# Optimization experiments

Hardware: AMD Instinct MI355X
Metric: run time of the kernel (lower is better)

Reference implementation:

```python
import jax, jax.numpy as jnp
import numpy as np

D_HID = 512
N_HEADS = 16
D_HEAD = D_HID // N_HEADS  # 32
D_FFN = 2048
B, N = 4, 1024
FACTOR = 0.5 / np.sqrt(D_HEAD)
EPS = 1e-5


def layer_norm(x, g, b):
    m = x.mean(-1, keepdims=True)
    v = ((x - m) ** 2).mean(-1, keepdims=True)
    return (x - m) / jnp.sqrt(v + EPS) * g + b


def setup_inputs() -> dict:
    key = jax.random.key(0)
    ks = jax.random.split(key, 24)
    s = 0.02
    p = lambda k, shape: jax.random.normal(k, shape, jnp.float32) * s
    inp = {
        'H': jax.random.normal(ks[0], (B, N, D_HID), jnp.float32),
        'V': jax.random.normal(ks[1], (B, N, 3, D_HID), jnp.float32),
        'D_batch': jax.random.normal(ks[2], (B, N, N), jnp.float32),
        'rbf_bias': jax.random.normal(ks[3], (B, 1, N, N), jnp.float32),
        'H_mask': jax.random.randint(ks[4], (B, N), 0, 2, jnp.int32),
        # attention sublayer params
        'g1': jnp.ones((D_HID,), jnp.float32), 'beta1': jnp.zeros((D_HID,), jnp.float32),
        'Wq': p(ks[5], (D_HID, 4 * D_HID)), 'bq': p(ks[6], (4 * D_HID,)),
        'Wk': p(ks[7], (D_HID, 4 * D_HID)), 'bk': p(ks[8], (4 * D_HID,)),
        'Wv': p(ks[9], (D_HID, D_HID)), 'bv': p(ks[10], (D_HID,)),
        'Wvv': p(ks[11], (D_HID, D_HID)),
        'Wo': p(ks[12], (D_HID, D_HID)), 'bo': p(ks[13], (D_HID,)),
        'Wvo': p(ks[14], (D_HID, D_HID)),
        # GVP FFN sublayer params
        'g2': jnp.ones((D_HID,), jnp.float32), 'beta2': jnp.zeros((D_HID,), jnp.float32),
        'Wlv': p(ks[15], (D_HID, 2 * D_HID)),
        'W1': p(ks[16], (2 * D_HID, D_FFN)), 'b1f': p(ks[17], (D_FFN,)),
        'W2': p(ks[18], (D_FFN, 2 * D_HID)), 'b2f': p(ks[19], (2 * D_HID,)),
    }
    return inp


def ept_forward(H, V, D_batch, rbf_bias, H_mask, g1, beta1, Wq, bq, Wk, bk, Wv, bv,
                Wvv, Wo, bo, Wvo, g2, beta2, Wlv, W1, b1f, W2, b2f):
    b, n, d = H.shape
    # ---- attention sublayer (pre-LN on H only, residual on H and V) ----
    Hn = layer_norm(H, g1, beta1)
    Hq = (Hn @ Wq + bq).reshape(b, n, N_HEADS, 4 * D_HEAD)
    Hk = (Hn @ Wk + bk).reshape(b, n, N_HEADS, 4 * D_HEAD)
    Hv = (Hn @ Wv + bv).reshape(b, n, N_HEADS, D_HEAD)
    # vector values: [b,n,3,d] -> [b,n,heads,3*dh]
    Vv = (V @ Wvv).reshape(b, n, 3, N_HEADS, D_HEAD).transpose(0, 1, 3, 2, 4)
    Vv = Vv.reshape(b, n, N_HEADS, 3 * D_HEAD)
    V_attn = jnp.concatenate([Hv, Vv], axis=-1)  # [b,n,h,4*dh]
    bias = rbf_bias + D_batch[:, None]  # [b,1,n,n]
    keep = (H_mask != 0)[:, None, None, :]  # mask keys
    bias = jnp.where(keep, bias, -jnp.inf)
    logits = jnp.einsum('bnhd,bmhd->bhnm', Hq, Hk) * FACTOR + bias
    attn = jax.nn.softmax(logits, axis=-1)
    res = jnp.einsum('bhnm,bmhd->bnhd', attn, V_attn)  # [b,n,h,4*dh]
    H_res = res[..., :D_HEAD].reshape(b, n, d)
    V_res = res[..., D_HEAD:].reshape(b, n, N_HEADS, 3, D_HEAD)
    V_res = V_res.transpose(0, 1, 3, 2, 4).reshape(b, n, 3, d)
    H = H + H_res @ Wo + bo
    V = V + V_res @ Wvo
    # ---- GVP FFN sublayer (pre-LN on H only, residual) ----
    Hn2 = layer_norm(H, g2, beta2)
    Vp = V @ Wlv  # [b,n,3,2d]
    V1, V2 = Vp[..., :d], Vp[..., d:]
    scaler = jnp.concatenate([Hn2, jnp.sqrt((V1 ** 2).sum(axis=-2))], axis=-1)
    h = jax.nn.silu(scaler @ W1 + b1f) @ W2 + b2f  # [b,n,2d]
    H = H + h[..., :d]
    V = V + h[..., None, d:] * V2
    return H, V


def reference(H, V, D_batch, rbf_bias, H_mask, g1, beta1, Wq, bq, Wk, bk, Wv, bv,
              Wvv, Wo, bo, Wvo, g2, beta2, Wlv, W1, b1f, W2, b2f):
    return ept_forward(H, V, D_batch, rbf_bias, H_mask, g1, beta1, Wq, bq, Wk, bk,
                       Wv, bv, Wvv, Wo, bo, Wvo, g2, beta2, Wlv, W1, b1f, W2, b2f)
```

## Files before the change

kernel.cpp:

```cpp
#include <hip/hip_runtime.h>
#include <math.h>

#define NBATCH 4
#define NSEQ   1024
#define DHID   512
#define NHEADS 16
#define ROWS   (NBATCH*NSEQ)
#define VROWS  (ROWS*3)
#define ATT_FACTOR 0.08838834764831845f
#define LOG2E 1.4426950408889634f
#define F2 (ATT_FACTOR*LOG2E)
#define SM_SHIFT (16.0f*LOG2E)

typedef __attribute__((ext_vector_type(8))) short short8;
typedef __attribute__((ext_vector_type(4))) float floatx4;

#define AS1 __attribute__((address_space(1)))
#define AS3 __attribute__((address_space(3)))
#define GLOAD_LDS16(g, l) \
  __builtin_amdgcn_global_load_lds((const AS1 void*)(g), (AS3 void*)(l), 16, 0, 0)

__device__ __forceinline__ ushort f2bf(float x) {
  union { float f; unsigned u; } v; v.f = x;
  unsigned r = v.u + 0x7fff + ((v.u >> 16) & 1);
  return (ushort)(r >> 16);
}
__device__ __forceinline__ float bf2f(ushort u) {
  union { unsigned u; float f; } v; v.u = ((unsigned)u) << 16; return v.f;
}

template<int OBF>
__global__ __launch_bounds__(256) void ln_kernel(
    const float* __restrict__ x, void* __restrict__ y, int ystride,
    const float* __restrict__ g, const float* __restrict__ beta)
{
  int row = blockIdx.x;
  int t = threadIdx.x;
  const float* xr = x + (size_t)row * DHID;
  float2 v = ((const float2*)xr)[t];
  float s  = v.x + v.y;
  float ss = v.x*v.x + v.y*v.y;
  #pragma unroll
  for (int off = 32; off > 0; off >>= 1) {
    s  += __shfl_down(s, off);
    ss += __shfl_down(ss, off);
  }
  __shared__ float red[8];
  int w = t >> 6;
  if ((t & 63) == 0) { red[w*2] = s; red[w*2+1] = ss; }
  __syncthreads();
  s  = red[0] + red[2] + red[4] + red[6];
  ss = red[1] + red[3] + red[5] + red[7];
  float mean = s * (1.0f/DHID);
  float var  = ss * (1.0f/DHID) - mean*mean;
  float rstd = rsqrtf(var + 1e-5f);
  float2 gg = ((const float2*)g)[t];
  float2 bb = ((const float2*)beta)[t];
  float2 o;
  o.x = (v.x - mean) * rstd * gg.x + bb.x;
  o.y = (v.y - mean) * rstd * gg.y + bb.y;
  if constexpr (OBF) {
    ushort2 u = { f2bf(o.x), f2bf(o.y) };
    *(ushort2*)&((ushort*)y)[(size_t)row * ystride + 2*t] = u;
  } else {
    *(float2*)&((float*)y)[(size_t)row * ystride + 2*t] = o;
  }
}

struct WJobs {
  const float* src[9];
  ushort*      dst[9];
  int K[9];
  int N[9];
  int blk0[10];
};

__global__ __launch_bounds__(256) void wtrans_all_kernel(WJobs J)
{
  __shared__ float Ts[64][65];
  int bid = blockIdx.x;
  int j = 0;
  #pragma unroll
  for (int i = 1; i < 9; i++) if (bid >= J.blk0[i]) j = i;
  const float* W = J.src[j];
  ushort* Wt = J.dst[j];
  int K = J.K[j], N = J.N[j];
  int local = bid - J.blk0[j];
  int nx = N >> 6;
  int bx = local - (local / nx) * nx;
  int by = local / nx;
  int k0 = by*64, n0 = bx*64;
  int t = threadIdx.x;
  #pragma unroll
  for (int p = 0; p < 4; p++) {
    int f = p*256 + t;
    int r = f >> 4, c = (f & 15)*4;
    float4 v = *(const float4*)&W[(size_t)(k0+r)*N + n0 + c];
    Ts[r][c] = v.x; Ts[r][c+1] = v.y; Ts[r][c+2] = v.z; Ts[r][c+3] = v.w;
  }
  __syncthreads();
  #pragma unroll
  for (int p = 0; p < 2; p++) {
    int gidx = p*256 + t;
    int nr = gidx >> 3, kc = (gidx & 7)*8;
    ushort u[8];
    #pragma unroll
    for (int x = 0; x < 8; x++) u[x] = f2bf(Ts[kc+x][nr]);
    ushort4 a = {u[0],u[1],u[2],u[3]}, b4 = {u[4],u[5],u[6],u[7]};
    *(ushort4*)&Wt[(size_t)(n0+nr)*K + k0 + kc]     = a;
    *(ushort4*)&Wt[(size_t)(n0+nr)*K + k0 + kc + 4] = b4;
  }
}

__global__ __launch_bounds__(256) void conv_bf16_kernel(
    const float* __restrict__ x, ushort* __restrict__ y)
{
  int i = blockIdx.x*256 + threadIdx.x;
  float4 v = ((const float4*)x)[i];
  ushort4 u = { f2bf(v.x), f2bf(v.y), f2bf(v.z), f2bf(v.w) };
  ((ushort4*)y)[i] = u;
}

__global__ __launch_bounds__(256) void biascat_kernel(
    const float* __restrict__ bq, const float* __restrict__ bk,
    const float* __restrict__ bv, float* __restrict__ o)
{
  int i = blockIdx.x*256 + threadIdx.x;
  float v = (i < 2048) ? bq[i] : (i < 4096 ? bk[i-2048] : bv[i-4096]);
  o[i] = v;
}

template<int ACT, int HAS_BIAS, int HAS_RES, int OUT_BF16, int DUAL>
__global__ __launch_bounds__(256) void gemm_mfma_kernel(
    const ushort* __restrict__ A, const ushort* __restrict__ Bt,
    const float* __restrict__ bias, const float* __restrict__ resid,
    void* __restrict__ Cv, ushort* __restrict__ C2,
    int M, int N, int K)
{
  __shared__ ushort As[2][128*32];
  __shared__ ushort Bs[2][128*32];
  int t = threadIdx.x;
  int w = t >> 6, lane = t & 63;
  int q16 = lane & 15, quad = lane >> 4;
  int m0 = blockIdx.y * 128, n0 = blockIdx.x * 128;
  int wm = (w & 1) * 64, wn = (w >> 1) * 64;

  int r0 = t >> 2;
  int c0 = (t & 3) * 8;
  const ushort* Ag = A  + (size_t)(m0 + r0) * K + c0;
  const ushort* Bg = Bt + (size_t)(n0 + r0) * K + c0;
  int wb = w * 512;

  floatx4 acc[4][4];
  #pragma unroll
  for (int i = 0; i < 4; i++)
    #pragma unroll
    for (int j = 0; j < 4; j++) acc[i][j] = (floatx4){0.f,0.f,0.f,0.f};

  #define STAGE(buf, kk) do { \
    GLOAD_LDS16(Ag + (kk),                 &As[buf][wb]); \
    GLOAD_LDS16(Ag + (size_t)64*K + (kk),  &As[buf][2048 + wb]); \
    GLOAD_LDS16(Bg + (kk),                 &Bs[buf][wb]); \
    GLOAD_LDS16(Bg + (size_t)64*K + (kk),  &Bs[buf][2048 + wb]); \
  } while (0)

  STAGE(0, 0);
  __syncthreads();

  int nt = K >> 5;
  int cur = 0;
  for (int kt = 0; kt < nt; kt++) {
    if (kt + 1 < nt) STAGE(cur ^ 1, (kt + 1) * 32);
    short8 af[4], bf4[4];
    #pragma unroll
    for (int i = 0; i < 4; i++) {
      af[i]  = *(const short8*)&As[cur][(wm + i*16 + q16)*32 + quad*8];
      bf4[i] = *(const short8*)&Bs[cur][(wn + i*16 + q16)*32 + quad*8];
    }
    #pragma unroll
    for (int i = 0; i < 4; i++)
      #pragma unroll
      for (int j = 0; j < 4; j++)
        acc[i][j] = __builtin_amdgcn_mfma_f32_16x16x32_bf16(af[i], bf4[j], acc[i][j], 0, 0, 0);
    __syncthreads();
    cur ^= 1;
  }
  #undef STAGE

  float* Cf = (float*)Cv;
  ushort* Cu = (ushort*)Cv;
  float bj[4];
  #pragma unroll
  for (int j = 0; j < 4; j++)
    bj[j] = HAS_BIAS ? bias[n0 + wn + j*16 + q16] : 0.f;
  #pragma unroll
  for (int i = 0; i < 4; i++) {
    #pragma unroll
    for (int r = 0; r < 4; r++) {
      int row = m0 + wm + i*16 + quad*4 + r;
      size_t base = (size_t)row * N;
      #pragma unroll
      for (int j = 0; j < 4; j++) {
        int col = n0 + wn + j*16 + q16;
        float v = acc[i][j][r] + bj[j];
        if constexpr (ACT == 1) v = v / (1.f + __expf(-v));
        if constexpr (HAS_RES) v += resid[base + col];
        if constexpr (OUT_BF16) Cu[base + col] = f2bf(v);
        else                    Cf[base + col] = v;
        if constexpr (DUAL) C2[base + col] = f2bf(v);
      }
    }
  }
}

__global__ __launch_bounds__(256) void gemm_wovo_kernel(
    const ushort* __restrict__ A,
    const ushort* __restrict__ WoTp, const ushort* __restrict__ WvoTp,
    const float* __restrict__ bo,
    const float* __restrict__ Hres, const float* __restrict__ Vres,
    float* __restrict__ Hout, float* __restrict__ Vout,
    ushort* __restrict__ Voutbf)
{
  const int K = 512;
  __shared__ ushort As[2][128*32];
  __shared__ ushort Bs[2][128*32];
  int t = threadIdx.x;
  int w = t >> 6, lane = t & 63;
  int q16 = lane & 15, quad = lane >> 4;
  int m0 = blockIdx.y * 128, n0 = blockIdx.x * 128;
  int wm = (w & 1) * 64, wn = (w >> 1) * 64;
  bool inH = (m0 < 4096);
  const ushort* Bt = inH ? WoTp : WvoTp;

  int r0 = t >> 2;
  int c0 = (t & 3) * 8;
  const ushort* Ag = A  + (size_t)(m0 + r0) * K + c0;
  const ushort* Bg = Bt + (size_t)(n0 + r0) * K + c0;
  int wb = w * 512;

  floatx4 acc[4][4];
  #pragma unroll
  for (int i = 0; i < 4; i++)
    #pragma unroll
    for (int j = 0; j < 4; j++) acc[i][j] = (floatx4){0.f,0.f,0.f,0.f};

  #define STAGE(buf, kk) do { \
    GLOAD_LDS16(Ag + (kk),                 &As[buf][wb]); \
    GLOAD_LDS16(Ag + (size_t)64*K + (kk),  &As[buf][2048 + wb]); \
    GLOAD_LDS16(Bg + (kk),                 &Bs[buf][wb]); \
    GLOAD_LDS16(Bg + (size_t)64*K + (kk),  &Bs[buf][2048 + wb]); \
  } while (0)

  STAGE(0, 0);
  __syncthreads();

  int cur = 0;
  for (int kt = 0; kt < 16; kt++) {
    if (kt + 1 < 16) STAGE(cur ^ 1, (kt + 1) * 32);
    short8 af[4], bf4[4];
    #pragma unroll
    for (int i = 0; i < 4; i++) {
      af[i]  = *(const short8*)&As[cur][(wm + i*16 + q16)*32 + quad*8];
      bf4[i] = *(const short8*)&Bs[cur][(wn + i*16 + q16)*32 + quad*8];
    }
    #pragma unroll
    for (int i = 0; i < 4; i++)
      #pragma unroll
      for (int j = 0; j < 4; j++)
        acc[i][j] = __builtin_amdgcn_mfma_f32_16x16x32_bf16(af[i], bf4[j], acc[i][j], 0, 0, 0);
    __syncthreads();
    cur ^= 1;
  }
  #undef STAGE

  float bj[4];
  #pragma unroll
  for (int j = 0; j < 4; j++)
    bj[j] = inH ? bo[n0 + wn + j*16 + q16] : 0.f;
  #pragma unroll
  for (int i = 0; i < 4; i++) {
    #pragma unroll
    for (int r = 0; r < 4; r++) {
      int row = m0 + wm + i*16 + quad*4 + r;
      #pragma unroll
      for (int j = 0; j < 4; j++) {
        int col = n0 + wn + j*16 + q16;
        float v = acc[i][j][r] + bj[j];
        if (inH) {
          size_t idx = (size_t)row * 512 + col;
          Hout[idx] = v + Hres[idx];
        } else {
          size_t idx = (size_t)(row - 4096) * 512 + col;
          float vv = v + Vres[idx];
          Vout[idx] = vv;
          Voutbf[idx] = f2bf(vv);
        }
      }
    }
  }
}

__global__ __launch_bounds__(256) void gemm_w2_kernel(
    const ushort* __restrict__ A, const ushort* __restrict__ Bt,
    const float* __restrict__ bias, float* __restrict__ C)
{
  const int N = 1024, K = 2048;
  __shared__ ushort As[2][64*32];
  __shared__ ushort Bs[2][128*32];
  int t = threadIdx.x;
  int w = t >> 6, lane = t & 63;
  int q16 = lane & 15, quad = lane >> 4;
  int m0 = blockIdx.y * 64, n0 = blockIdx.x * 128;
  int wm = (w & 1) * 32, wn = (w >> 1) * 64;

  int r0 = t >> 2;
  int c0 = (t & 3) * 8;
  const ushort* Ag = A  + (size_t)(m0 + r0) * K + c0;
  const ushort* Bg = Bt + (size_t)(n0 + r0) * K + c0;
  int wb = w * 512;

  floatx4 acc[2][4];
  #pragma unroll
  for (int i = 0; i < 2; i++)
    #pragma unroll
    for (int j = 0; j < 4; j++) acc[i][j] = (floatx4){0.f,0.f,0.f,0.f};

  #define STAGE(buf, kk) do { \
    GLOAD_LDS16(Ag + (kk),                 &As[buf][wb]); \
    GLOAD_LDS16(Bg + (kk),                 &Bs[buf][wb]); \
    GLOAD_LDS16(Bg + (size_t)64*K + (kk),  &Bs[buf][2048 + wb]); \
  } while (0)

  STAGE(0, 0);
  __syncthreads();

  int cur = 0;
  for (int kt = 0; kt < 64; kt++) {
    if (kt + 1 < 64) STAGE(cur ^ 1, (kt + 1) * 32);
    short8 af[2], bf4[4];
    #pragma unroll
    for (int i = 0; i < 2; i++)
      af[i]  = *(const short8*)&As[cur][(wm + i*16 + q16)*32 + quad*8];
    #pragma unroll
    for (int j = 0; j < 4; j++)
      bf4[j] = *(const short8*)&Bs[cur][(wn + j*16 + q16)*32 + quad*8];
    #pragma unroll
    for (int i = 0; i < 2; i++)
      #pragma unroll
      for (int j = 0; j < 4; j++)
        acc[i][j] = __builtin_amdgcn_mfma_f32_16x16x32_bf16(af[i], bf4[j], acc[i][j], 0, 0, 0);
    __syncthreads();
    cur ^= 1;
  }
  #undef STAGE

  float bj[4];
  #pragma unroll
  for (int j = 0; j < 4; j++)
    bj[j] = bias[n0 + wn + j*16 + q16];
  #pragma unroll
  for (int i = 0; i < 2; i++) {
    #pragma unroll
    for (int r = 0; r < 4; r++) {
      int row = m0 + wm + i*16 + quad*4 + r;
      #pragma unroll
      for (int j = 0; j < 4; j++) {
        int col = n0 + wn + j*16 + q16;
        C[(size_t)row * N + col] = acc[i][j][r] + bj[j];
      }
    }
  }
}

__global__ __launch_bounds__(256) void bias2_kernel(
    const float* __restrict__ Db, const float* __restrict__ Rb,
    const int* __restrict__ Mask, ushort* __restrict__ Bc2)
{
  int i2 = blockIdx.x*256 + threadIdx.x;
  int e = i2 * 2;
  int b = e >> 20;
  int m = e & 1023;
  float2 d = *(const float2*)&Db[e];
  float2 r = *(const float2*)&Rb[e];
  ushort2 o;
  o.x = Mask[b*NSEQ + m]     ? f2bf((d.x + r.x)*LOG2E) : f2bf(-1e30f);
  o.y = Mask[b*NSEQ + m + 1] ? f2bf((d.y + r.y)*LOG2E) : f2bf(-1e30f);
  *(ushort2*)&Bc2[e] = o;
}

__global__ __launch_bounds__(256) void vtrans_kernel(
    const ushort* __restrict__ QKV, const ushort* __restrict__ VVr,
    ushort* __restrict__ Vt)
{
  __shared__ float Ts[64][33];
  int t = threadIdx.x;
  int bh = blockIdx.z;
  int b = bh >> 4, h = bh & 15;
  int dt = blockIdx.y;
  int nt = blockIdx.x;
  int d0 = dt*32, n0 = nt*64;
  #pragma unroll
  for (int i = 0; i < 2; i++) {
    int nl = (t >> 3) + i*32;
    int c4 = (t & 7)*4;
    const ushort* src;
    if (dt == 0) src = &QKV[(size_t)(b*NSEQ + n0 + nl)*4608 + 4096 + h*32 + c4];
    else { int c = dt - 1; src = &VVr[((size_t)(b*NSEQ + n0 + nl)*3 + c)*512 + h*32 + c4]; }
    ushort4 v = *(const ushort4*)src;
    Ts[nl][c4] = bf2f(v.x); Ts[nl][c4+1] = bf2f(v.y);
    Ts[nl][c4+2] = bf2f(v.z); Ts[nl][c4+3] = bf2f(v.w);
  }
  __syncthreads();
  int dl = t >> 3;
  int n8 = (t & 7)*8;
  ushort u[8];
  #pragma unroll
  for (int k = 0; k < 8; k++) u[k] = f2bf(Ts[n8+k][dl]);
  size_t ob = ((size_t)bh*128 + d0 + dl)*NSEQ + n0 + n8;
  ushort4 u0 = {u[0],u[1],u[2],u[3]}, u1 = {u[4],u[5],u[6],u[7]};
  *(ushort4*)&Vt[ob]     = u0;
  *(ushort4*)&Vt[ob + 4] = u1;
}

__global__ __launch_bounds__(256, 2) void attn_mfma_kernel(
    const ushort* __restrict__ QKV,
    const ushort* __restrict__ Vt, const ushort* __restrict__ Bc2,
    ushort* __restrict__ HRES, ushort* __restrict__ VRES)
{
  __shared__ union {
    ushort q[128][136];
    struct {
      ushort k[64][136];
      ushort v[128][72];
      ushort bias[128][72];
    } s;
  } S;
  __shared__ ushort Ps[4][32][72];

  int t = threadIdx.x;
  int w = t >> 6, lane = t & 63;
  int q16 = lane & 15, quad = lane >> 4;
  int h = blockIdx.x, qt = blockIdx.y, b = blockIdx.z;
  int q0 = qt * 128;

  float4 rk0, rk1, rk2, rk3;
  float4 rv0, rv1, rv2, rv3;
  float4 rb0, rb1, rb2, rb3;
  const size_t kbase = (size_t)(b*NSEQ)*4608 + 2048 + h*128 + (t&3)*8;
  const size_t vbase = ((size_t)(b*NHEADS + h)*128 + (t>>3))*NSEQ + (t&7)*8;
  const size_t bbase = (size_t)(b*NSEQ + q0 + (t>>3))*NSEQ + (t&7)*8;
  int kr = t >> 2;
  int kc = (t & 3)*8;
  int vr = t >> 3, vc = (t & 7)*8;

  #define LOADT(m0_) do { \
    const ushort* kp = &QKV[kbase + (size_t)((m0_) + kr)*4608]; \
    rk0 = *(const float4*)(kp +  0); \
    rk1 = *(const float4*)(kp + 32); \
    rk2 = *(const float4*)(kp + 64); \
    rk3 = *(const float4*)(kp + 96); \
    const ushort* vp = &Vt[vbase + (m0_)]; \
    rv0 = *(const float4*)(vp + (size_t) 0*NSEQ); \
    rv1 = *(const float4*)(vp + (size_t)32*NSEQ); \
    rv2 = *(const float4*)(vp + (size_t)64*NSEQ); \
    rv3 = *(const float4*)(vp + (size_t)96*NSEQ); \
    const ushort* bp2 = &Bc2[bbase + (m0_)]; \
    rb0 = *(const float4*)(bp2 + (size_t) 0*NSEQ); \
    rb1 = *(const float4*)(bp2 + (size_t)32*NSEQ); \
    rb2 = *(const float4*)(bp2 + (size_t)64*NSEQ); \
    rb3 = *(const float4*)(bp2 + (size_t)96*NSEQ); \
  } while (0)

  #define STORET() do { \
    *(float4*)&S.s.k[kr][kc +  0] = rk0; \
    *(float4*)&S.s.k[kr][kc + 32] = rk1; \
    *(float4*)&S.s.k[kr][kc + 64] = rk2; \
    *(float4*)&S.s.k[kr][kc + 96] = rk3; \
    *(float4*)&S.s.v[vr +  0][vc] = rv0; \
    *(float4*)&S.s.v[vr + 32][vc] = rv1; \
    *(float4*)&S.s.v[vr + 64][vc] = rv2; \
    *(float4*)&S.s.v[vr + 96][vc] = rv3; \
    *(float4*)&S.s.bias[vr +  0][vc] = rb0; \
    *(float4*)&S.s.bias[vr + 32][vc] = rb1; \
    *(float4*)&S.s.bias[vr + 64][vc] = rb2; \
    *(float4*)&S.s.bias[vr + 96][vc] = rb3; \
  } while (0)

  LOADT(0);

  #pragma unroll
  for (int i = 0; i < 8; i++) {
    int f = t + i*256;
    int r = f >> 4, c8 = f & 15;
    *(float4*)&S.q[r][c8*8] =
        *(const float4*)&QKV[(size_t)(b*NSEQ + q0 + r)*4608 + h*128 + c8*8];
  }
  __syncthreads();
  short8 qf[2][4];
  #pragma unroll
  for (int rg = 0; rg < 2; rg++)
    #pragma unroll
    for (int c = 0; c < 4; c++)
      qf[rg][c] = *(const short8*)&S.q[w*32 + rg*16 + q16][c*32 + quad*8];

  floatx4 o[2][8];
  #pragma unroll
  for (int rg = 0; rg < 2; rg++)
    #pragma unroll
    for (int i = 0; i < 8; i++) o[rg][i] = (floatx4){0.f,0.f,0.f,0.f};
  float l_i[2] = {0.f, 0.f};

  #pragma unroll 1
  for (int it = 0; it < 16; it++) {
    __syncthreads();
    STORET();
    if (it < 15) LOADT((it + 1) * 64);
    __syncthreads();

    floatx4 sf[2][4];
    #pragma unroll
    for (int rg = 0; rg < 2; rg++)
      #pragma unroll
      for (int g = 0; g < 4; g++) sf[rg][g] = (floatx4){0.f,0.f,0.f,0.f};
    __builtin_amdgcn_s_setprio(1);
    #pragma unroll
    for (int c = 0; c < 4; c++) {
      short8 kf[4];
      #pragma unroll
      for (int g = 0; g < 4; g++)
        kf[g] = *(const short8*)&S.s.k[g*16 + q16][c*32 + quad*8];
      #pragma unroll
      for (int rg = 0; rg < 2; rg++)
        #pragma unroll
        for (int g = 0; g < 4; g++)
          sf[rg][g] = __builtin_amdgcn_mfma_f32_16x16x32_bf16(kf[g], qf[rg][c], sf[rg][g], 0, 0, 0);
    }
    __builtin_amdgcn_s_setprio(0);

    #pragma unroll
    for (int rg = 0; rg < 2; rg++) {
      int brow = w*32 + rg*16 + q16;
      #pragma unroll
      for (int g = 0; g < 4; g++) {
        ushort4 bb = *(const ushort4*)&S.s.bias[brow][g*16 + quad*4];
        float p0 = exp2f(sf[rg][g][0]*F2 + bf2f(bb.x) - SM_SHIFT);
        float p1 = exp2f(sf[rg][g][1]*F2 + bf2f(bb.y) - SM_SHIFT);
        float p2 = exp2f(sf[rg][g][2]*F2 + bf2f(bb.z) - SM_SHIFT);
        float p3 = exp2f(sf[rg][g][3]*F2 + bf2f(bb.w) - SM_SHIFT);
        l_i[rg] += (p0 + p1) + (p2 + p3);
        unsigned d0, d1;
        asm("v_cvt_pk_bf16_f32 %0, %1, %2" : "=v"(d0) : "v"(p0), "v"(p1));
        asm("v_cvt_pk_bf16_f32 %0, %1, %2" : "=v"(d1) : "v"(p2), "v"(p3));
        uint2 dd = { d0, d1 };
        *(uint2*)&Ps[w][rg*16 + q16][g*16 + quad*4] = dd;
      }
    }

    short8 pf[2][2];
    #pragma unroll
    for (int rg = 0; rg < 2; rg++)
      #pragma unroll
      for (int ks = 0; ks < 2; ks++)
        pf[rg][ks] = *(const short8*)&Ps[w][rg*16 + q16][ks*32 + quad*8];
    __builtin_amdgcn_s_setprio(1);
    #pragma unroll
    for (int tt = 0; tt < 8; tt++) {
      short8 vf0 = *(const short8*)&S.s.v[tt*16 + q16][quad*8];
      short8 vf1 = *(const short8*)&S.s.v[tt*16 + q16][32 + quad*8];
      #pragma unroll
      for (int rg = 0; rg < 2; rg++) {
        o[rg][tt] = __builtin_amdgcn_mfma_f32_16x16x32_bf16(pf[rg][0], vf0, o[rg][tt], 0, 0, 0);
        o[rg][tt] = __builtin_amdgcn_mfma_f32_16x16x32_bf16(pf[rg][1], vf1, o[rg][tt], 0, 0, 0);
      }
    }
    __builtin_amdgcn_s_setprio(0);
  }
  #undef LOADT
  #undef STORET

  #pragma unroll
  for (int rg = 0; rg < 2; rg++) {
    float l = l_i[rg];
    l += __shfl_xor(l, 16);
    l += __shfl_xor(l, 32);
    #pragma unroll
    for (int i = 0; i < 4; i++) {
      float li = __shfl(l, quad*4 + i);
      float inv = 1.0f / li;
      int grow = b*NSEQ + q0 + w*32 + rg*16 + quad*4 + i;
      #pragma unroll
      for (int tt = 0; tt < 2; tt++)
        HRES[(size_t)grow*512 + h*32 + tt*16 + q16] = f2bf(o[rg][tt][i] * inv);
      #pragma unroll
      for (int tt = 2; tt < 8; tt++) {
        int c = (tt - 2) >> 1;
        int jj = ((tt - 2) & 1)*16 + q16;
        VRES[((size_t)grow*3 + c)*512 + h*32 + jj] = f2bf(o[rg][tt][i] * inv);
      }
    }
  }
}

__global__ __launch_bounds__(256) void vnorm_kernel(
    const float* __restrict__ VP, ushort* __restrict__ SC)
{
  int idx = blockIdx.x*256 + threadIdx.x;
  int row = idx >> 9;
  int d = idx & 511;
  const float* p = VP + (size_t)row*3072 + d;
  float a = p[0], b = p[1024], c = p[2048];
  SC[(size_t)row*1024 + 512 + d] = f2bf(sqrtf(a*a + b*b + c*c));
}

__global__ __launch_bounds__(256) void finale_kernel(
    const float* __restrict__ HH, const float* __restrict__ VP,
    float* __restrict__ Hout, float* __restrict__ Vout)
{
  int idx = blockIdx.x*256 + threadIdx.x;
  if (idx < ROWS*DHID) {
    int row = idx >> 9;
    int d = idx & 511;
    Hout[idx] += HH[(size_t)row*1024 + d];
  } else {
    int k = idx - ROWS*DHID;
    int r3 = k >> 9;
    int d = k & 511;
    int row = r3 / 3;
    Vout[k] += HH[(size_t)row*1024 + 512 + d] * VP[(size_t)r3*1024 + 512 + d];
  }
}

extern "C" void kernel_launch(void* const* d_in, const int* in_sizes, int n_in,
                              void* d_out, int out_size, void* d_ws, size_t ws_size,
                              hipStream_t stream)
{
  const float* H    = (const float*)d_in[0];
  const float* V    = (const float*)d_in[1];
  const float* Db   = (const float*)d_in[2];
  const float* Rb   = (const float*)d_in[3];
  const int*   Mask = (const int*)d_in[4];
  const float* g1   = (const float*)d_in[5];
  const float* be1  = (const float*)d_in[6];
  const float* Wq   = (const float*)d_in[7];
  const float* bq   = (const float*)d_in[8];
  const float* Wk   = (const float*)d_in[9];
  const float* bkk  = (const float*)d_in[10];
  const float* Wv   = (const float*)d_in[11];
  const float* bv   = (const float*)d_in[12];
  const float* Wvv  = (const float*)d_in[13];
  const float* Wo   = (const float*)d_in[14];
  const float* bo   = (const float*)d_in[15];
  const float* Wvo  = (const float*)d_in[16];
  const float* g2   = (const float*)d_in[17];
  const float* be2  = (const float*)d_in[18];
  const float* Wlv  = (const float*)d_in[19];
  const float* W1   = (const float*)d_in[20];
  const float* b1f  = (const float*)d_in[21];
  const float* W2   = (const float*)d_in[22];
  const float* b2f  = (const float*)d_in[23];

  float* Hout = (float*)d_out;
  float* Vout = Hout + (size_t)ROWS*DHID;

  char* w = (char*)d_ws;
  const size_t MB = 1024*1024;
  const size_t KB = 1024;
  ushort* WqT  = (ushort*)(w + 0);
  ushort* WkT  = (ushort*)(w + 2048*KB);
  ushort* WvT  = (ushort*)(w + 4096*KB);
  ushort* WvvT = (ushort*)(w + 4608*KB);
  ushort* WoT  = (ushort*)(w + 5120*KB);
  ushort* WvoT = (ushort*)(w + 5632*KB);
  ushort* WlvT = (ushort*)(w + 6144*KB);
  ushort* W1T  = (ushort*)(w + 7168*KB);
  ushort* W2T  = (ushort*)(w + 11264*KB);
  float*  Bqkv = (float*)(w + 15360*KB);
  ushort* HNbf  = (ushort*)(w + 16*MB);
  ushort* QKVbf = (ushort*)(w + 20*MB);
  ushort* VVrbf = (ushort*)(w + 56*MB);
  ushort* Vbf   = (ushort*)(w + 68*MB);
  ushort* Vtb   = (ushort*)(w + 80*MB);
  ushort* Bc2   = (ushort*)(w + 96*MB);
  ushort* HRESbf = (ushort*)(w + 104*MB);
  ushort* VRESbf = (ushort*)(w + 108*MB);
  ushort* Voutbf = (ushort*)(w + 20*MB);
  float*  VP     = (float*)(w + 56*MB);
  ushort* SCbf   = (ushort*)(w + 104*MB);
  ushort* S1bf   = (ushort*)(w + 112*MB);
  float*  HHb    = (float*)(w + 32*MB);

  dim3 blk(256);

  WJobs J;
  const float* ws_[9] = {Wq, Wk, Wv, Wvv, Wo, Wvo, Wlv, W1, W2};
  ushort* wd_[9] = {WqT, WkT, WvT, WvvT, WoT, WvoT, WlvT, W1T, W2T};
  int wk_[9] = {512, 512, 512, 512, 512, 512, 512, 1024, 2048};
  int wn_[9] = {2048, 2048, 512, 512, 512, 512, 1024, 2048, 1024};
  int off = 0;
  for (int i = 0; i < 9; i++) {
    J.src[i] = ws_[i]; J.dst[i] = wd_[i]; J.K[i] = wk_[i]; J.N[i] = wn_[i];
    J.blk0[i] = off;
    off += (wn_[i] >> 6) * (wk_[i] >> 6);
  }
  J.blk0[9] = off;
  wtrans_all_kernel<<<off, blk, 0, stream>>>(J);

  ln_kernel<1><<<ROWS, blk, 0, stream>>>(H, HNbf, DHID, g1, be1);
  conv_bf16_kernel<<<(VROWS*DHID/4)/256, blk, 0, stream>>>(V, Vbf);
  biascat_kernel<<<18, blk, 0, stream>>>(bq, bkk, bv, Bqkv);

  gemm_mfma_kernel<0,1,0,1,0><<<dim3(36, 32), blk, 0, stream>>>(HNbf, WqT, Bqkv, nullptr, QKVbf, nullptr, 4096, 4608, 512);
  gemm_mfma_kernel<0,0,0,1,0><<<dim3( 4, 96), blk, 0, stream>>>(Vbf, WvvT, nullptr, nullptr, VVrbf, nullptr, 12288, 512, 512);

  bias2_kernel<<<(NBATCH*NSEQ*NSEQ/2)/256, blk, 0, stream>>>(Db, Rb, Mask, Bc2);
  vtrans_kernel<<<dim3(16, 4, 64), blk, 0, stream>>>(QKVbf, VVrbf, Vtb);

  attn_mfma_kernel<<<dim3(16, 8, 4), blk, 0, stream>>>(QKVbf, Vtb, Bc2, HRESbf, VRESbf);

  gemm_wovo_kernel<<<dim3(4, 128), blk, 0, stream>>>(HRESbf, WoT, WvoT, bo, H, V, Hout, Vout, Voutbf);

  ln_kernel<1><<<ROWS, blk, 0, stream>>>(Hout, SCbf, 1024, g2, be2);
  gemm_mfma_kernel<0,0,0,0,0><<<dim3(8, 96), blk, 0, stream>>>(Voutbf, WlvT, nullptr, nullptr, VP, nullptr, 12288, 1024, 512);
  vnorm_kernel<<<(ROWS*DHID)/256, blk, 0, stream>>>(VP, SCbf);

  gemm_mfma_kernel<1,1,0,1,0><<<dim3(16, 32), blk, 0, stream>>>(SCbf, W1T, b1f, nullptr, S1bf, nullptr, 4096, 2048, 1024);
  gemm_w2_kernel<<<dim3(8, 64), blk, 0, stream>>>(S1bf, W2T, b2f, HHb);
  finale_kernel<<<((ROWS + VROWS)*DHID)/256, blk, 0, stream>>>(HHb, VP, Hout, Vout);
}
```

Before: 468.0 us.

## Triple-buffer GEMM K-tiles and load attention bias directly into registers

The three MFMA GEMM kernels move from double to triple buffering. Each now prefetches two K-tiles ahead and replaces __syncthreads with explicit vmcnt/lgkmcnt waits plus a raw barrier, so global-to-LDS loads can stay in flight across iterations. The attention kernel stops staging the bias tile through LDS, reads it straight from global memory into registers, and shrinks the LDS padding, which lowers LDS traffic and footprint. The trade-offs are more LDS use in the GEMMs, which may reduce occupancy, and hand-counted waitcnt values that must match the number of outstanding loads exactly.

```diff
diff --git a/kernel.cpp b/kernel.cpp
--- a/kernel.cpp
+++ b/kernel.cpp
@@ -19,6 +19,12 @@
 #define AS3 __attribute__((address_space(3)))
 #define GLOAD_LDS16(g, l) \
   __builtin_amdgcn_global_load_lds((const AS1 void*)(g), (AS3 void*)(l), 16, 0, 0)
+
+#define WAIT_VM4_LGKM0() asm volatile("s_waitcnt vmcnt(4) lgkmcnt(0)" ::: "memory")
+#define WAIT_VM3_LGKM0() asm volatile("s_waitcnt vmcnt(3) lgkmcnt(0)" ::: "memory")
+#define WAIT_VM0_LGKM0() asm volatile("s_waitcnt vmcnt(0) lgkmcnt(0)" ::: "memory")
+#define WAIT_LGKM0()     asm volatile("s_waitcnt lgkmcnt(0)" ::: "memory")
+#define BARRIER()        __builtin_amdgcn_s_barrier()
 
 __device__ __forceinline__ ushort f2bf(float x) {
   union { float f; unsigned u; } v; v.f = x;
@@ -137,8 +143,8 @@
     void* __restrict__ Cv, ushort* __restrict__ C2,
     int M, int N, int K)
 {
-  __shared__ ushort As[2][128*32];
-  __shared__ ushort Bs[2][128*32];
+  __shared__ ushort As[3][128*32];
+  __shared__ ushort Bs[3][128*32];
   int t = threadIdx.x;
   int w = t >> 6, lane = t & 63;
   int q16 = lane & 15, quad = lane >> 4;
@@ -157,20 +163,23 @@
     #pragma unroll
     for (int j = 0; j < 4; j++) acc[i][j] = (floatx4){0.f,0.f,0.f,0.f};
 
-  #define STAGE(buf, kk) do { \
-    GLOAD_LDS16(Ag + (kk),                 &As[buf][wb]); \
-    GLOAD_LDS16(Ag + (size_t)64*K + (kk),  &As[buf][2048 + wb]); \
-    GLOAD_LDS16(Bg + (kk),                 &Bs[buf][wb]); \
-    GLOAD_LDS16(Bg + (size_t)64*K + (kk),  &Bs[buf][2048 + wb]); \
+  #define STAGE(ab, bb2, kk) do { \
+    GLOAD_LDS16(Ag + (kk),                 (ab) + wb); \
+    GLOAD_LDS16(Ag + (size_t)64*K + (kk),  (ab) + 2048 + wb); \
+    GLOAD_LDS16(Bg + (kk),                 (bb2) + wb); \
+    GLOAD_LDS16(Bg + (size_t)64*K + (kk),  (bb2) + 2048 + wb); \
   } while (0)
 
-  STAGE(0, 0);
-  __syncthreads();
-
   int nt = K >> 5;
-  int cur = 0;
+  STAGE(As[0], Bs[0], 0);
+  STAGE(As[1], Bs[1], 32);
+  WAIT_VM4_LGKM0();
+  BARRIER();
+
+  int cur = 0, nxt = 1, pre = 2;
   for (int kt = 0; kt < nt; kt++) {
-    if (kt + 1 < nt) STAGE(cur ^ 1, (kt + 1) * 32);
+    bool more = (kt + 2 < nt);
+    if (more) STAGE(As[pre], Bs[pre], (kt + 2) * 32);
     short8 af[4], bf4[4];
     #pragma unroll
     for (int i = 0; i < 4; i++) {
@@ -182,8 +191,10 @@
       #pragma unroll
       for (int j = 0; j < 4; j++)
         acc[i][j] = __builtin_amdgcn_mfma_f32_16x16x32_bf16(af[i], bf4[j], acc[i][j], 0, 0, 0);
-    __syncthreads();
-    cur ^= 1;
+    if (more) WAIT_VM4_LGKM0();
+    else      WAIT_VM0_LGKM0();
+    BARRIER();
+    int tmp = cur; cur = nxt; nxt = pre; pre = tmp;
   }
   #undef STAGE
 
@@ -222,8 +233,8 @@
     ushort* __restrict__ Voutbf)
 {
   const int K = 512;
-  __shared__ ushort As[2][128*32];
-  __shared__ ushort Bs[2][128*32];
+  __shared__ ushort As[3][128*32];
+  __shared__ ushort Bs[3][128*32];
   int t = threadIdx.x;
   int w = t >> 6, lane = t & 63;
   int q16 = lane & 15, quad = lane >> 4;
@@ -244,19 +255,22 @@
     #pragma unroll
     for (int j = 0; j < 4; j++) acc[i][j] = (floatx4){0.f,0.f,0.f,0.f};
 
-  #define STAGE(buf, kk) do { \
-    GLOAD_LDS16(Ag + (kk),                 &As[buf][wb]); \
-    GLOAD_LDS16(Ag + (size_t)64*K + (kk),  &As[buf][2048 + wb]); \
-    GLOAD_LDS16(Bg + (kk),                 &Bs[buf][wb]); \
-    GLOAD_LDS16(Bg + (size_t)64*K + (kk),  &Bs[buf][2048 + wb]); \
+  #define STAGE(ab, bb2, kk) do { \
+    GLOAD_LDS16(Ag + (kk),                 (ab) + wb); \
+    GLOAD_LDS16(Ag + (size_t)64*K + (kk),  (ab) + 2048 + wb); \
+    GLOAD_LDS16(Bg + (kk),                 (bb2) + wb); \
+    GLOAD_LDS16(Bg + (size_t)64*K + (kk),  (bb2) + 2048 + wb); \
   } while (0)
 
-  STAGE(0, 0);
-  __syncthreads();
-
-  int cur = 0;
+  STAGE(As[0], Bs[0], 0);
+  STAGE(As[1], Bs[1], 32);
+  WAIT_VM4_LGKM0();
+  BARRIER();
+
+  int cur = 0, nxt = 1, pre = 2;
   for (int kt = 0; kt < 16; kt++) {
-    if (kt + 1 < 16) STAGE(cur ^ 1, (kt + 1) * 32);
+    bool more = (kt + 2 < 16);
+    if (more) STAGE(As[pre], Bs[pre], (kt + 2) * 32);
     short8 af[4], bf4[4];
     #pragma unroll
     for (int i = 0; i < 4; i++) {
@@ -268,8 +282,10 @@
       #pragma unroll
       for (int j = 0; j < 4; j++)
         acc[i][j] = __builtin_amdgcn_mfma_f32_16x16x32_bf16(af[i], bf4[j], acc[i][j], 0, 0, 0);
-    __syncthreads();
-    cur ^= 1;
+    if (more) WAIT_VM4_LGKM0();
+    else      WAIT_VM0_LGKM0();
+    BARRIER();
+    int tmp = cur; cur = nxt; nxt = pre; pre = tmp;
   }
   #undef STAGE
 
@@ -305,8 +321,8 @@
     const float* __restrict__ bias, float* __restrict__ C)
 {
   const int N = 1024, K = 2048;
-  __shared__ ushort As[2][64*32];
-  __shared__ ushort Bs[2][128*32];
+  __shared__ ushort As[3][64*32];
+  __shared__ ushort Bs[3][128*32];
   int t = threadIdx.x;
   int w = t >> 6, lane = t & 63;
   int q16 = lane & 15, quad = lane >> 4;
@@ -325,18 +341,21 @@
     #pragma unroll
     for (int j = 0; j < 4; j++) acc[i][j] = (floatx4){0.f,0.f,0.f,0.f};
 
-  #define STAGE(buf, kk) do { \
-    GLOAD_LDS16(Ag + (kk),                 &As[buf][wb]); \
-    GLOAD_LDS16(Bg + (kk),                 &Bs[buf][wb]); \
-    GLOAD_LDS16(Bg + (size_t)64*K + (kk),  &Bs[buf][2048 + wb]); \
+  #define STAGE(ab, bb2, kk) do { \
+    GLOAD_LDS16(Ag + (kk),                 (ab) + wb); \
+    GLOAD_LDS16(Bg + (kk),                 (bb2) + wb); \
+    GLOAD_LDS16(Bg + (size_t)64*K + (kk),  (bb2) + 2048 + wb); \
   } while (0)
 
-  STAGE(0, 0);
-  __syncthreads();
-
-  int cur = 0;
+  STAGE(As[0], Bs[0], 0);
+  STAGE(As[1], Bs[1], 32);
+  WAIT_VM3_LGKM0();
+  BARRIER();
+
+  int cur = 0, nxt = 1, pre = 2;
   for (int kt = 0; kt < 64; kt++) {
-    if (kt + 1 < 64) STAGE(cur ^ 1, (kt + 1) * 32);
+    bool more = (kt + 2 < 64);
+    if (more) STAGE(As[pre], Bs[pre], (kt + 2) * 32);
     short8 af[2], bf4[4];
     #pragma unroll
     for (int i = 0; i < 2; i++)
@@ -349,8 +368,10 @@
       #pragma unroll
       for (int j = 0; j < 4; j++)
         acc[i][j] = __builtin_amdgcn_mfma_f32_16x16x32_bf16(af[i], bf4[j], acc[i][j], 0, 0, 0);
-    __syncthreads();
-    cur ^= 1;
+    if (more) WAIT_VM3_LGKM0();
+    else      WAIT_VM0_LGKM0();
+    BARRIER();
+    int tmp = cur; cur = nxt; nxt = pre; pre = tmp;
   }
   #undef STAGE
 
@@ -428,11 +449,10 @@
     ushort* __restrict__ HRES, ushort* __restrict__ VRES)
 {
   __shared__ union {
-    ushort q[128][136];
+    ushort q[128][132];
     struct {
-      ushort k[64][136];
-      ushort v[128][72];
-      ushort bias[128][72];
+      ushort k[64][132];
+      ushort v[128][68];
     } s;
   } S;
   __shared__ ushort Ps[4][32][72];
@@ -445,13 +465,13 @@
 
   float4 rk0, rk1, rk2, rk3;
   float4 rv0, rv1, rv2, rv3;
-  float4 rb0, rb1, rb2, rb3;
   const size_t kbase = (size_t)(b*NSEQ)*4608 + 2048 + h*128 + (t&3)*8;
   const size_t vbase = ((size_t)(b*NHEADS + h)*128 + (t>>3))*NSEQ + (t&7)*8;
-  const size_t bbase = (size_t)(b*NSEQ + q0 + (t>>3))*NSEQ + (t&7)*8;
   int kr = t >> 2;
   int kc = (t & 3)*8;
   int vr = t >> 3, vc = (t & 7)*8;
+  const ushort* Br0 = Bc2 + (size_t)(b*NSEQ + q0 + w*32 + q16)*NSEQ;
+  const ushort* Br1 = Br0 + (size_t)16*NSEQ;
 
   #define LOADT(m0_) do { \
     const ushort* kp = &QKV[kbase + (size_t)((m0_) + kr)*4608]; \
@@ -464,11 +484,6 @@
     rv1 = *(const float4*)(vp + (size_t)32*NSEQ); \
     rv2 = *(const float4*)(vp + (size_t)64*NSEQ); \
     rv3 = *(const float4*)(vp + (size_t)96*NSEQ); \
-    const ushort* bp2 = &Bc2[bbase + (m0_)]; \
-    rb0 = *(const float4*)(bp2 + (size_t) 0*NSEQ); \
-    rb1 = *(const float4*)(bp2 + (size_t)32*NSEQ); \
-    rb2 = *(const float4*)(bp2 + (size_t)64*NSEQ); \
-    rb3 = *(const float4*)(bp2 + (size_t)96*NSEQ); \
   } while (0)
 
   #define STORET() do { \
@@ -480,10 +495,6 @@
     *(float4*)&S.s.v[vr + 32][vc] = rv1; \
     *(float4*)&S.s.v[vr + 64][vc] = rv2; \
     *(float4*)&S.s.v[vr + 96][vc] = rv3; \
-    *(float4*)&S.s.bias[vr +  0][vc] = rb0; \
-    *(float4*)&S.s.bias[vr + 32][vc] = rb1; \
-    *(float4*)&S.s.bias[vr + 64][vc] = rb2; \
-    *(float4*)&S.s.bias[vr + 96][vc] = rb3; \
   } while (0)
 
   LOADT(0);
@@ -512,10 +523,21 @@
 
   #pragma unroll 1
   for (int it = 0; it < 16; it++) {
-    __syncthreads();
+    WAIT_LGKM0();
+    BARRIER();
     STORET();
+    int mb = it*64 + quad*4;
+    ushort4 bbv[2][4];
+    #pragma unroll
+    for (int rg = 0; rg < 2; rg++) {
+      const ushort* br = rg ? Br1 : Br0;
+      #pragma unroll
+      for (int g = 0; g < 4; g++)
+        bbv[rg][g] = *(const ushort4*)&br[mb + g*16];
+    }
     if (it < 15) LOADT((it + 1) * 64);
-    __syncthreads();
+    WAIT_LGKM0();
+    BARRIER();
 
     floatx4 sf[2][4];
     #pragma unroll
@@ -539,10 +561,9 @@
 
     #pragma unroll
     for (int rg = 0; rg < 2; rg++) {
-      int brow = w*32 + rg*16 + q16;
       #pragma unroll
       for (int g = 0; g < 4; g++) {
-        ushort4 bb = *(const ushort4*)&S.s.bias[brow][g*16 + quad*4];
+        ushort4 bb = bbv[rg][g];
         float p0 = exp2f(sf[rg][g][0]*F2 + bf2f(bb.x) - SM_SHIFT);
         float p1 = exp2f(sf[rg][g][1]*F2 + bf2f(bb.y) - SM_SHIFT);
         float p2 = exp2f(sf[rg][g][2]*F2 + bf2f(bb.z) - SM_SHIFT);
```

New measurement: 549.8 us. +17.5%, slower.
